# Kernel tuning notes

Measured on AMD Instinct MI355X. Metric: run time of the kernel, lower is better.

The kernel has to match this reference:

```python
import jax, jax.numpy as jnp
import numpy as np

B, S, DIM = 2, 2048, 1024
H, DH = 16, 64  # num_head, head_dim


def setup_inputs() -> dict:
    key = jax.random.key(0)
    ks = jax.random.split(key, 9)
    s = 1.0 / np.sqrt(DIM)
    s2 = 1.0 / np.sqrt(H * DH)
    return {
        "X": jax.random.normal(ks[0], (B, S, DIM), dtype=jnp.float32),
        "mask": jnp.ones((B, S), dtype=jnp.float32),
        "Wq": jax.random.normal(ks[1], (DIM, H * DH), dtype=jnp.float32) * s,
        "bq": jax.random.normal(ks[2], (H * DH,), dtype=jnp.float32) * s,
        "Wk": jax.random.normal(ks[3], (DIM, H * DH), dtype=jnp.float32) * s,
        "bk": jax.random.normal(ks[4], (H * DH,), dtype=jnp.float32) * s,
        "Wv": jax.random.normal(ks[5], (DIM, H * DH), dtype=jnp.float32) * s,
        "bv": jax.random.normal(ks[6], (H * DH,), dtype=jnp.float32) * s,
        "Wo": jax.random.normal(ks[7], (H * DH, DIM), dtype=jnp.float32) * s2,
        "bo": jax.random.normal(ks[8], (DIM,), dtype=jnp.float32) * s2,
    }


def _split_heads(x):
    # [B,S,H*DH] -> [B,H,S,DH]
    return x.reshape(B, S, H, DH).transpose(0, 2, 1, 3)


def reference(X, mask, Wq, bq, Wk, bk, Wv, bv, Wo, bo):
    Q = _split_heads(X @ Wq + bq)
    K = _split_heads(X @ Wk + bk)
    V = _split_heads(X @ Wv + bv)
    # scores: [B,H,S,S]
    dot = jnp.einsum("bhqd,bhkd->bhqk", Q, K) / np.sqrt(DH).astype(np.float32)
    dot = dot - 1000000.0 * (1.0 - mask[:, None, None, :])
    attn = jax.nn.softmax(dot, axis=-1)
    ctx = jnp.einsum("bhqk,bhkd->bhqd", attn, V)
    # combine heads: [B,S,H*DH]
    ctx = ctx.transpose(0, 2, 1, 3).reshape(B, S, H * DH)
    return ctx @ Wo + bo
```

## Files before the change

kernel.cpp:

```cpp
#include <hip/hip_runtime.h>
#include <hip/hip_bf16.h>
#include <math.h>

#define BB 2
#define SS 2048
#define DIM 1024
#define NH 16
#define DH 64

typedef __bf16 bf16x8 __attribute__((ext_vector_type(8)));
typedef float f32x4 __attribute__((ext_vector_type(4)));
typedef float f32x16 __attribute__((ext_vector_type(16)));
typedef unsigned int u32x4 __attribute__((ext_vector_type(4)));

#define PENL2 (1000000.0f * 1.44269504f)

__device__ __forceinline__ void glds16(const __hip_bfloat16* g, __hip_bfloat16* l) {
    __builtin_amdgcn_global_load_lds(
        (const __attribute__((address_space(1))) void*)g,
        (__attribute__((address_space(3))) void*)l, 16, 0, 0);
}

__device__ __forceinline__ unsigned short f2bf(float x) {
    unsigned int u = __builtin_bit_cast(unsigned int, x);
    return (unsigned short)((u + 0x8000u) >> 16);
}

__device__ __forceinline__ unsigned int pk2bf(float a, float b) {
#if __has_builtin(__builtin_amdgcn_cvt_pk_bf16_f32)
    typedef __bf16 bf16x2 __attribute__((ext_vector_type(2)));
    bf16x2 p = __builtin_amdgcn_cvt_pk_bf16_f32(a, b);
    return __builtin_bit_cast(unsigned int, p);
#else
    return (unsigned int)f2bf(a) | ((unsigned int)f2bf(b) << 16);
#endif
}

__device__ __forceinline__ float fexp2(float x) {
#if __has_builtin(__builtin_amdgcn_exp2f)
    return __builtin_amdgcn_exp2f(x);
#else
    return exp2f(x);
#endif
}

__global__ void prep(const float* __restrict__ X,
                     const float* __restrict__ Wq, const float* __restrict__ Wk,
                     const float* __restrict__ Wv, const float* __restrict__ Wo,
                     const float* __restrict__ mask, float* __restrict__ pf,
                     __hip_bfloat16* __restrict__ T4, ushort4* __restrict__ Xbf) {
    int z = blockIdx.z;
    int t = threadIdx.x;
    if (z == 4) {
        int c = blockIdx.y * 32 + blockIdx.x;
        const float4* in = (const float4*)X;
#pragma unroll
        for (int k = 0; k < 4; ++k) {
            int i = c * 1024 + k * 256 + t;
            float4 v = in[i];
            ushort4 h;
            h.x = f2bf(v.x); h.y = f2bf(v.y); h.z = f2bf(v.z); h.w = f2bf(v.w);
            Xbf[i] = h;
        }
        if (c < 16) {
            int i = c * 256 + t;
            pf[i] = -PENL2 * (1.0f - mask[i]);
        }
        return;
    }
    const float* W = (z == 0) ? Wq : (z == 1) ? Wk : (z == 2) ? Wv : Wo;
    __hip_bfloat16* Thi = T4 + (size_t)z * DIM * DIM;
    __shared__ float tile[32][33];
    int k0 = blockIdx.x * 32, n0 = blockIdx.y * 32;
    int r = t >> 3, c = (t & 7) << 2;
    float4 v = *(const float4*)&W[(size_t)(k0 + r) * DIM + n0 + c];
    tile[r][c] = v.x; tile[r][c + 1] = v.y; tile[r][c + 2] = v.z; tile[r][c + 3] = v.w;
    __syncthreads();
    size_t base = (size_t)(n0 + r) * DIM + k0 + c;
#pragma unroll
    for (int i = 0; i < 4; ++i)
        ((unsigned short*)Thi)[base + i] = f2bf(tile[c + i][r]);
}

#define BM 128
#define BN 128
#define BK 32
#define QSCALE (0.125f * 1.44269504f)
__global__ __launch_bounds__(256) void gemm_bf(
    const __hip_bfloat16* __restrict__ A, const __hip_bfloat16* __restrict__ B,
    const float* __restrict__ b0, const float* __restrict__ b1, const float* __restrict__ b2,
    __hip_bfloat16* __restrict__ oq, __hip_bfloat16* __restrict__ ok,
    __hip_bfloat16* __restrict__ ov, float* __restrict__ of32, int mode) {
    __shared__ alignas(16) __hip_bfloat16 sA[2][BM * BK];
    __shared__ alignas(16) __hip_bfloat16 sB[2][BN * BK];
    const int K = 1024;
    int tid = threadIdx.x;
    int wave = tid >> 6, lane = tid & 63, quad = lane >> 4, l16 = lane & 15;

    int nbx = gridDim.x;
    int nwg = nbx * gridDim.y;
    int bid = blockIdx.y * nbx + blockIdx.x;
    int swz = (bid & 7) * (nwg >> 3) + (bid >> 3);
    int m0 = (swz / nbx) * BM, n0 = (swz % nbx) * BN;
    int mo = (wave >> 1) * 64, no = (wave & 1) * 64;

    f32x4 acc[4][4];
#pragma unroll
    for (int i = 0; i < 4; ++i)
#pragma unroll
        for (int j = 0; j < 4; ++j) acc[i][j] = (f32x4){0.f, 0.f, 0.f, 0.f};

    int ar = tid >> 2;
    int ac = (tid & 3) << 3;
    const __hip_bfloat16* gA = A + (size_t)(m0 + ar) * K + ac;
    const __hip_bfloat16* gB = B + (size_t)(n0 + ar) * K + ac;

    auto STG = [&](int bb, int k0) {
        glds16(gA + k0, &sA[bb][ar * BK + ac]);
        glds16(gA + (size_t)64 * K + k0, &sA[bb][(ar + 64) * BK + ac]);
        glds16(gB + k0, &sB[bb][ar * BK + ac]);
        glds16(gB + (size_t)64 * K + k0, &sB[bb][(ar + 64) * BK + ac]);
    };

    STG(0, 0);
    int cur = 0;
    for (int k0 = 0; k0 < K; k0 += BK) {
        __syncthreads();
        if (k0 + BK < K) STG(cur ^ 1, k0 + BK);

        bf16x8 a_h[4], b_h[4];
#pragma unroll
        for (int i = 0; i < 4; ++i)
            a_h[i] = *(const bf16x8*)&sA[cur][(mo + i * 16 + l16) * BK + quad * 8];
#pragma unroll
        for (int j = 0; j < 4; ++j)
            b_h[j] = *(const bf16x8*)&sB[cur][(no + j * 16 + l16) * BK + quad * 8];
#pragma unroll
        for (int i = 0; i < 4; ++i)
#pragma unroll
            for (int j = 0; j < 4; ++j)
                acc[i][j] = __builtin_amdgcn_mfma_f32_16x16x32_bf16(a_h[i], b_h[j], acc[i][j], 0, 0, 0);
        cur ^= 1;
    }

    int which = (mode == 1) ? (n0 >> 10) : 0;
    const float* bp = (mode == 0) ? b0 : (which == 0) ? b0 : (which == 1) ? b1 : b2;
#pragma unroll
    for (int i = 0; i < 4; ++i)
#pragma unroll
        for (int j = 0; j < 4; ++j) {
            int gmb = m0 + mo + i * 16 + quad * 4;
            int gn  = n0 + no + j * 16 + l16;
            int nn  = gn & 1023;
            float bb = bp[(mode == 0) ? gn : nn];
#pragma unroll
            for (int r = 0; r < 4; ++r) {
                int gm = gmb + r;
                float v = acc[i][j][r] + bb;
                if (mode == 0) {
                    of32[(size_t)gm * 1024 + gn] = v;
                } else {
                    int b = gm >> 11, s = gm & 2047, h = nn >> 6, d = nn & 63;
                    if (which == 0)
                        ((unsigned short*)oq)[(((size_t)(b * NH + h)) * SS + s) * DH + d] = f2bf(v * QSCALE);
                    else if (which == 1)
                        ((unsigned short*)ok)[(((size_t)(b * NH + h)) * SS + s) * DH + d] = f2bf(v);
                    else
                        ((unsigned short*)ov)[(((size_t)(b * NH + h)) * DH + d) * SS + s] = f2bf(v);
                }
            }
        }
}

__global__ __launch_bounds__(256, 4) void flash_split(
        const __hip_bfloat16* __restrict__ Q,
        const __hip_bfloat16* __restrict__ K,
        const __hip_bfloat16* __restrict__ Vt,
        const float* __restrict__ pf,
        __hip_bfloat16* __restrict__ Op0, __hip_bfloat16* __restrict__ Op1,
        float* __restrict__ lp0, float* __restrict__ lp1) {
    int bh = blockIdx.y;
    int b = bh >> 4, h = bh & (NH - 1);
    int q0 = blockIdx.x * 128;
    int z  = blockIdx.z;
    __hip_bfloat16* Op = z ? Op1 : Op0;
    float*          lp = z ? lp1 : lp0;
    int tid = threadIdx.x;
    int wave = tid >> 6, lane = tid & 63;
    int l31 = lane & 31, hi = lane >> 5, l7 = lane & 7;

    __shared__ alignas(16) __hip_bfloat16 sK[2][64 * 64];
    __shared__ alignas(16) __hip_bfloat16 sV[2][64 * 64];

    const __hip_bfloat16* Qrow = Q + ((size_t)bh * SS + q0 + wave * 32 + l31) * DH;
    bf16x8 aq[4];
#pragma unroll
    for (int d_ = 0; d_ < 4; ++d_)
        aq[d_] = *(const bf16x8*)(Qrow + d_ * 16 + 8 * hi);

    const __hip_bfloat16* Kb = K + (size_t)bh * SS * DH;
    const __hip_bfloat16* Vb = Vt + (size_t)bh * DH * SS;
    const float* pfb = pf + b * SS;

    f32x16 z16;
#pragma unroll
    for (int r = 0; r < 16; ++r) z16[r] = 0.f;
    f32x16 O[2];
    O[0] = z16; O[1] = z16;
    f32x4 ls = (f32x4){0.f, 0.f, 0.f, 0.f};

    int xo[4];
#pragma unroll
    for (int c = 0; c < 4; ++c) xo[c] = ((((c << 1) | hi) ^ l7) << 4);

    int r8 = lane >> 3, c8 = lane & 7;
    int ck = c8 ^ r8;

    const int kbeg = z * (SS / 2);
    const int NT = (SS / 2) / 64;

    auto STAGE = [&](int bb, int k0) {
#pragma unroll
        for (int cc = 0; cc < 2; ++cc) {
            int row = cc * 32 + wave * 8 + r8;
            glds16(Kb + (size_t)(k0 + row) * DH + ck * 8, &sK[bb][row * 64 + c8 * 8]);
            glds16(Vb + (size_t)row * SS + k0 + ck * 8,  &sV[bb][row * 64 + c8 * 8]);
        }
    };

    STAGE(0, kbeg);
    __syncthreads();
    int cur = 0;
    for (int t = 0; t < NT; ++t) {
        int k0 = kbeg + t * 64;
        if (t + 1 < NT) STAGE(cur ^ 1, k0 + 64);
        const float* pfk = pfb + k0;
#pragma unroll
        for (int tt = 0; tt < 2; ++tt) {
            const char* pK = (const char*)&sK[cur][(tt * 32 + l31) * 64];
            bf16x8 kf[4];
#pragma unroll
            for (int d_ = 0; d_ < 4; ++d_)
                kf[d_] = *(const bf16x8*)(pK + xo[d_]);
            f32x16 st;
#pragma unroll
            for (int g = 0; g < 4; ++g) {
                f32x4 pv = *(const f32x4*)&pfk[32 * tt + 8 * g + 4 * hi];
#pragma unroll
                for (int j = 0; j < 4; ++j) st[4 * g + j] = pv[j];
            }
            __builtin_amdgcn_s_setprio(1);
#pragma unroll
            for (int d_ = 0; d_ < 4; ++d_)
                st = __builtin_amdgcn_mfma_f32_32x32x16_bf16(kf[d_], aq[d_], st, 0, 0, 0);
            __builtin_amdgcn_s_setprio(0);

#pragma unroll
            for (int g = 0; g < 4; ++g) {
#pragma unroll
                for (int j = 0; j < 4; ++j)
                    st[4 * g + j] = fexp2(st[4 * g + j]);
                ls[0] += st[4 * g];     ls[1] += st[4 * g + 1];
                ls[2] += st[4 * g + 2]; ls[3] += st[4 * g + 3];
            }

            unsigned int u[8];
#pragma unroll
            for (int g = 0; g < 4; ++g) {
                u[2 * g]     = pk2bf(st[4 * g],     st[4 * g + 1]);
                u[2 * g + 1] = pk2bf(st[4 * g + 2], st[4 * g + 3]);
            }

#pragma unroll
            for (int kk = 0; kk < 2; ++kk) {
                unsigned int w0 = u[4 * kk],     w2 = u[4 * kk + 2];
                unsigned int w1 = u[4 * kk + 1], w3 = u[4 * kk + 3];
                asm("v_permlane32_swap_b32 %0, %1" : "+v"(w0), "+v"(w2));
                asm("v_permlane32_swap_b32 %0, %1" : "+v"(w1), "+v"(w3));
                u32x4 paw; paw.x = w0; paw.y = w1; paw.z = w2; paw.w = w3;
                bf16x8 pa = __builtin_bit_cast(bf16x8, paw);
                int ks = 2 * tt + kk;
                __builtin_amdgcn_s_setprio(1);
#pragma unroll
                for (int dt_ = 0; dt_ < 2; ++dt_) {
                    const char* pV = (const char*)&sV[cur][(dt_ * 32 + l31) * 64];
                    bf16x8 vf = *(const bf16x8*)(pV + xo[ks]);
                    O[dt_] = __builtin_amdgcn_mfma_f32_32x32x16_bf16(pa, vf, O[dt_], 0, 0, 0);
                }
                __builtin_amdgcn_s_setprio(0);
            }
        }
        __syncthreads();
        cur ^= 1;
    }

    unsigned short* op = (unsigned short*)Op;
    int qb = q0 + wave * 32;
#pragma unroll
    for (int dt_ = 0; dt_ < 2; ++dt_)
#pragma unroll
        for (int r = 0; r < 16; ++r) {
            int qq = (r & 3) + 8 * (r >> 2) + 4 * hi;
            op[((size_t)b * SS + qb + qq) * (NH * DH) + h * DH + dt_ * 32 + l31] =
                f2bf(O[dt_][r]);
        }
    float lt = ls[0] + ls[1] + ls[2] + ls[3];
    lt += __shfl_xor(lt, 32, 64);
    if (hi == 0)
        lp[(size_t)bh * SS + qb + l31] = lt;
}

__global__ __launch_bounds__(256) void combine(
        const __hip_bfloat16* __restrict__ O1, const __hip_bfloat16* __restrict__ O2,
        const float* __restrict__ l1, const float* __restrict__ l2,
        __hip_bfloat16* __restrict__ ctx) {
    int i = blockIdx.x * 256 + threadIdx.x;
    size_t base = (size_t)i * 8;
    int row = i >> 7;
    int h   = (i >> 3) & 15;
    int b = row >> 11, s = row & 2047;
    size_t bhq = ((size_t)(b * NH + h)) * SS + s;
    float linv = 1.0f / (l1[bhq] + l2[bhq]);
    bf16x8 a = *(const bf16x8*)(O1 + base);
    bf16x8 c = *(const bf16x8*)(O2 + base);
    ushort4 o0, o1;
    o0.x = f2bf(((float)a[0] + (float)c[0]) * linv);
    o0.y = f2bf(((float)a[1] + (float)c[1]) * linv);
    o0.z = f2bf(((float)a[2] + (float)c[2]) * linv);
    o0.w = f2bf(((float)a[3] + (float)c[3]) * linv);
    o1.x = f2bf(((float)a[4] + (float)c[4]) * linv);
    o1.y = f2bf(((float)a[5] + (float)c[5]) * linv);
    o1.z = f2bf(((float)a[6] + (float)c[6]) * linv);
    o1.w = f2bf(((float)a[7] + (float)c[7]) * linv);
    ((ushort4*)(ctx + base))[0] = o0;
    ((ushort4*)(ctx + base + 4))[0] = o1;
}

extern "C" void kernel_launch(void* const* d_in, const int* in_sizes, int n_in,
                              void* d_out, int out_size, void* d_ws, size_t ws_size,
                              hipStream_t stream) {
    const float* X    = (const float*)d_in[0];
    const float* mask = (const float*)d_in[1];
    const float* Wq   = (const float*)d_in[2];
    const float* bq   = (const float*)d_in[3];
    const float* Wk   = (const float*)d_in[4];
    const float* bk   = (const float*)d_in[5];
    const float* Wv   = (const float*)d_in[6];
    const float* bv   = (const float*)d_in[7];
    const float* Wo   = (const float*)d_in[8];
    const float* bo   = (const float*)d_in[9];
    float* out = (float*)d_out;

    const size_t MB = 1u << 20;
    char* ws = (char*)d_ws;
    __hip_bfloat16* Xbf = (__hip_bfloat16*)(ws);
    __hip_bfloat16* Op0 = (__hip_bfloat16*)(ws + 8 * MB);
    __hip_bfloat16* Wt4 = (__hip_bfloat16*)(ws + 16 * MB);
    float*          lp0 = (float*)(ws + 24 * MB);
    float*          lp1 = (float*)(ws + 25 * MB);
    float*          pf  = (float*)(ws + 26 * MB);
    __hip_bfloat16* Qw  = (__hip_bfloat16*)(ws + 32 * MB);
    __hip_bfloat16* Kw  = (__hip_bfloat16*)(ws + 40 * MB);
    __hip_bfloat16* Vt  = (__hip_bfloat16*)(ws + 48 * MB);
    __hip_bfloat16* Op1 = (__hip_bfloat16*)(ws + 56 * MB);
    __hip_bfloat16* Wot = Wt4 + (size_t)3 * DIM * DIM;

    dim3 pgrd(32, 32, 5);
    prep<<<pgrd, 256, 0, stream>>>(X, Wq, Wk, Wv, Wo, mask, pf, Wt4, (ushort4*)Xbf);

    dim3 qkvgrd(3 * DIM / BN, (BB * SS) / BM);
    gemm_bf<<<qkvgrd, 256, 0, stream>>>(Xbf, Wt4, bq, bk, bv,
                                        Qw, Kw, Vt, nullptr, 1);

    dim3 agrd(SS / 128, BB * NH, 2);
    flash_split<<<agrd, 256, 0, stream>>>(Qw, Kw, Vt, pf, Op0, Op1, lp0, lp1);

    combine<<<dim3(2048), 256, 0, stream>>>(Op0, Op1, lp0, lp1, Xbf);

    dim3 ogrd(DIM / BN, (BB * SS) / BM);
    gemm_bf<<<ogrd, 256, 0, stream>>>(Xbf, Wot, bo, nullptr, nullptr,
                                      nullptr, nullptr, nullptr, out, 0);
}
```

Baseline: 218.4 us.

## Restructure bf16 GEMM to 512 threads with triple-buffered LDS and swizzle

The projection GEMM now runs 8 waves per 128x128 tile, each computing 64x32, with a 3-stage LDS ring filled by global_load_lds. It waits with explicit vmcnt counters instead of a syncthreads per step. LDS columns are XOR-swizzled to avoid bank conflicts, and MFMA issue is wrapped in s_setprio. The goal is better latency hiding and higher occupancy, at the cost of more LDS per block, a second barrier per iteration, and hand-tuned wait counts that must match the number of outstanding loads.

After: 213.9 us. -2.0%, faster.

```diff
diff --git a/kernel.cpp b/kernel.cpp
--- a/kernel.cpp
+++ b/kernel.cpp
@@ -14,6 +14,8 @@
 typedef unsigned int u32x4 __attribute__((ext_vector_type(4)));
 
 #define PENL2 (1000000.0f * 1.44269504f)
+
+#define VMW(N) asm volatile("s_waitcnt vmcnt(" #N ")" ::: "memory")
 
 __device__ __forceinline__ void glds16(const __hip_bfloat16* g, __hip_bfloat16* l) {
     __builtin_amdgcn_global_load_lds(
@@ -86,13 +88,13 @@
 #define BN 128
 #define BK 32
 #define QSCALE (0.125f * 1.44269504f)
-__global__ __launch_bounds__(256) void gemm_bf(
+__global__ __launch_bounds__(512, 6) void gemm_bf(
     const __hip_bfloat16* __restrict__ A, const __hip_bfloat16* __restrict__ B,
     const float* __restrict__ b0, const float* __restrict__ b1, const float* __restrict__ b2,
     __hip_bfloat16* __restrict__ oq, __hip_bfloat16* __restrict__ ok,
     __hip_bfloat16* __restrict__ ov, float* __restrict__ of32, int mode) {
-    __shared__ alignas(16) __hip_bfloat16 sA[2][BM * BK];
-    __shared__ alignas(16) __hip_bfloat16 sB[2][BN * BK];
+    __shared__ alignas(16) __hip_bfloat16 sA[3][BM * BK];
+    __shared__ alignas(16) __hip_bfloat16 sB[3][BN * BK];
     const int K = 1024;
     int tid = threadIdx.x;
     int wave = tid >> 6, lane = tid & 63, quad = lane >> 4, l16 = lane & 15;
@@ -102,45 +104,64 @@
     int bid = blockIdx.y * nbx + blockIdx.x;
     int swz = (bid & 7) * (nwg >> 3) + (bid >> 3);
     int m0 = (swz / nbx) * BM, n0 = (swz % nbx) * BN;
-    int mo = (wave >> 1) * 64, no = (wave & 1) * 64;
-
-    f32x4 acc[4][4];
+    int mo = (wave >> 2) * 64, no = (wave & 3) * 32;
+
+    f32x4 acc[4][2];
 #pragma unroll
     for (int i = 0; i < 4; ++i)
 #pragma unroll
-        for (int j = 0; j < 4; ++j) acc[i][j] = (f32x4){0.f, 0.f, 0.f, 0.f};
+        for (int j = 0; j < 2; ++j) acc[i][j] = (f32x4){0.f, 0.f, 0.f, 0.f};
 
     int ar = tid >> 2;
-    int ac = (tid & 3) << 3;
-    const __hip_bfloat16* gA = A + (size_t)(m0 + ar) * K + ac;
-    const __hip_bfloat16* gB = B + (size_t)(n0 + ar) * K + ac;
+    int c4 = tid & 3;
+    int cs = c4 ^ ((ar >> 1) & 3);
+    const __hip_bfloat16* gA = A + (size_t)(m0 + ar) * K + cs * 8;
+    const __hip_bfloat16* gB = B + (size_t)(n0 + ar) * K + cs * 8;
+    int ldst = ar * BK + c4 * 8;
 
     auto STG = [&](int bb, int k0) {
-        glds16(gA + k0, &sA[bb][ar * BK + ac]);
-        glds16(gA + (size_t)64 * K + k0, &sA[bb][(ar + 64) * BK + ac]);
-        glds16(gB + k0, &sB[bb][ar * BK + ac]);
-        glds16(gB + (size_t)64 * K + k0, &sB[bb][(ar + 64) * BK + ac]);
+        glds16(gA + k0, &sA[bb][ldst]);
+        glds16(gB + k0, &sB[bb][ldst]);
     };
 
     STG(0, 0);
+    STG(1, BK);
     int cur = 0;
-    for (int k0 = 0; k0 < K; k0 += BK) {
-        __syncthreads();
-        if (k0 + BK < K) STG(cur ^ 1, k0 + BK);
-
-        bf16x8 a_h[4], b_h[4];
+    for (int it = 0; it < 32; ++it) {
+        int k0 = it * BK;
+        if (it < 30) {
+            int nb = cur + 2; if (nb >= 3) nb -= 3;
+            STG(nb, k0 + 2 * BK);
+            VMW(4);
+        } else if (it == 30) {
+            VMW(2);
+        } else {
+            VMW(0);
+        }
+        __builtin_amdgcn_s_barrier();
+
+        bf16x8 a_h[4], b_h[2];
+#pragma unroll
+        for (int i = 0; i < 4; ++i) {
+            int rr = mo + i * 16 + l16;
+            int ph = quad ^ ((rr >> 1) & 3);
+            a_h[i] = *(const bf16x8*)&sA[cur][rr * BK + ph * 8];
+        }
+#pragma unroll
+        for (int j = 0; j < 2; ++j) {
+            int rr = no + j * 16 + l16;
+            int ph = quad ^ ((rr >> 1) & 3);
+            b_h[j] = *(const bf16x8*)&sB[cur][rr * BK + ph * 8];
+        }
+        __builtin_amdgcn_s_setprio(1);
 #pragma unroll
         for (int i = 0; i < 4; ++i)
-            a_h[i] = *(const bf16x8*)&sA[cur][(mo + i * 16 + l16) * BK + quad * 8];
-#pragma unroll
-        for (int j = 0; j < 4; ++j)
-            b_h[j] = *(const bf16x8*)&sB[cur][(no + j * 16 + l16) * BK + quad * 8];
-#pragma unroll
-        for (int i = 0; i < 4; ++i)
-#pragma unroll
-            for (int j = 0; j < 4; ++j)
+#pragma unroll
+            for (int j = 0; j < 2; ++j)
                 acc[i][j] = __builtin_amdgcn_mfma_f32_16x16x32_bf16(a_h[i], b_h[j], acc[i][j], 0, 0, 0);
-        cur ^= 1;
+        __builtin_amdgcn_s_setprio(0);
+        __builtin_amdgcn_s_barrier();
+        cur = (cur == 2) ? 0 : cur + 1;
     }
 
     int which = (mode == 1) ? (n0 >> 10) : 0;
@@ -148,7 +169,7 @@
 #pragma unroll
     for (int i = 0; i < 4; ++i)
 #pragma unroll
-        for (int j = 0; j < 4; ++j) {
+        for (int j = 0; j < 2; ++j) {
             int gmb = m0 + mo + i * 16 + quad * 4;
             int gn  = n0 + no + j * 16 + l16;
             int nn  = gn & 1023;
@@ -369,7 +390,7 @@
     prep<<<pgrd, 256, 0, stream>>>(X, Wq, Wk, Wv, Wo, mask, pf, Wt4, (ushort4*)Xbf);
 
     dim3 qkvgrd(3 * DIM / BN, (BB * SS) / BM);
-    gemm_bf<<<qkvgrd, 256, 0, stream>>>(Xbf, Wt4, bq, bk, bv,
+    gemm_bf<<<qkvgrd, 512, 0, stream>>>(Xbf, Wt4, bq, bk, bv,
                                         Qw, Kw, Vt, nullptr, 1);
 
     dim3 agrd(SS / 128, BB * NH, 2);
@@ -378,6 +399,6 @@
     combine<<<dim3(2048), 256, 0, stream>>>(Op0, Op1, lp0, lp1, Xbf);
 
     dim3 ogrd(DIM / BN, (BB * SS) / BM);
-    gemm_bf<<<ogrd, 256, 0, stream>>>(Xbf, Wot, bo, nullptr, nullptr,
+    gemm_bf<<<ogrd, 512, 0, stream>>>(Xbf, Wot, bo, nullptr, nullptr,
                                       nullptr, nullptr, nullptr, out, 0);
 }
```
